# Performance work log

Measured on AMD Instinct MI355X. Metric: run time of the kernel, lower is better.

The kernel has to match this reference:

```python
import jax, jax.numpy as jnp
import numpy as np

N_NODES = 50000
N_EDGES = 800000
IN_C = 128
OUT_C = 128
NEG_SLOPE = 0.2  # leaky_relu alpha


def setup_inputs() -> dict:
    key = jax.random.key(0)
    k1, k2, k3, k4 = jax.random.split(key, 4)
    h = jax.random.normal(k1, (N_NODES, IN_C), dtype=jnp.float32)
    edge_index = jax.random.randint(k2, (2, N_EDGES), 0, N_NODES, dtype=jnp.int64)
    # xavier_uniform with gain=1.414
    gW = 1.414 * np.sqrt(6.0 / (IN_C + OUT_C))
    W = jax.random.uniform(k3, (IN_C, OUT_C), dtype=jnp.float32, minval=-gW, maxval=gW)
    ga = 1.414 * np.sqrt(6.0 / (2 * OUT_C + 1))
    a = jax.random.uniform(k4, (2 * OUT_C, 1), dtype=jnp.float32, minval=-ga, maxval=ga)
    return {"h": h, "edge_index": edge_index, "W": W, "a": a}


def reference(h, edge_index, W, a):
    # eval mode (no dropout), concat=True -> ELU output
    Wh = h @ W                                  # [N, F]
    row, col = edge_index[0], edge_index[1]     # source, target
    F_out = W.shape[1]
    # cat([Wh_i, Wh_j]) @ a  ==  (Wh @ a_src)[row] + (Wh @ a_dst)[col]
    alpha_src = Wh @ a[:F_out, 0]               # [N]
    alpha_dst = Wh @ a[F_out:, 0]               # [N]
    edge_e = jax.nn.leaky_relu(alpha_src[row] + alpha_dst[col], negative_slope=NEG_SLOPE)  # [E]
    n = Wh.shape[0]
    # segment softmax over incoming edges of each target node
    m = jax.ops.segment_max(edge_e, col, num_segments=n)       # [N] (-inf for empty, never indexed)
    exp_e = jnp.exp(edge_e - m[col])                            # [E]
    s = jax.ops.segment_sum(exp_e, col, num_segments=n)         # [N]
    attn = exp_e / (s[col] + 1e-16)                              # [E]
    # scatter-add aggregation of attended source features
    h_prime = jax.ops.segment_sum(Wh[row] * attn[:, None], col, num_segments=n)  # [N, F]
    return jax.nn.elu(h_prime)
```

## Files before the change

### kernel.cpp

```cpp
#include <hip/hip_runtime.h>
#include <math.h>

#define NEG_BIG -1.0e30f
#define BSHIFT 8
#define MAXB 256

typedef __attribute__((ext_vector_type(8))) short short8v;
typedef __attribute__((ext_vector_type(4))) float f32x4;

__device__ __forceinline__ ushort f2bf(float f) {
  unsigned u = __float_as_uint(f);
  unsigned r = (u + 0x7fffu + ((u >> 16) & 1u)) >> 16;
  return (ushort)r;
}
__device__ __forceinline__ float bf_lo(unsigned u) { return __uint_as_float(u << 16); }
__device__ __forceinline__ float bf_hi(unsigned u) { return __uint_as_float(u & 0xffff0000u); }

__global__ void wprep_k(const float* __restrict__ W, ushort* __restrict__ Wbf,
                        int* __restrict__ bucket_count, int* __restrict__ done) {
  int j = blockIdx.x * blockDim.x + threadIdx.x;
  if (j < MAXB) bucket_count[j] = 0;
  if (j == 0) *done = 0;
  if (j >= 128 * 128) return;
  int i = j & 7;
  int l = (j >> 3) & 63;
  int n0 = (j >> 9) & 7;
  int kk = j >> 12;
  int k = kk * 32 + ((l >> 4) & 3) * 8 + i;
  int n = n0 * 16 + (l & 15);
  Wbf[j] = f2bf(W[k * 128 + n]);
}

__global__ __launch_bounds__(256) void hist_gemm_k(
    const void* __restrict__ ei, int E,
    unsigned* __restrict__ packed, int* __restrict__ bucket_count,
    int* __restrict__ done, int* __restrict__ bcur, int* __restrict__ bucket_base,
    int hblocks,
    const float* __restrict__ h, const ushort* __restrict__ Wbf,
    const float* __restrict__ a, ushort* __restrict__ Whb,
    float* __restrict__ asrc, float* __restrict__ adst, int N) {
  __shared__ int lh[MAXB];
  __shared__ int wsum[4];
  __shared__ int last;
  int tid = (int)threadIdx.x;

  if ((int)blockIdx.x < hblocks) {
    lh[tid] = 0;
    __syncthreads();

    const int* p32 = (const int*)ei;
    bool is64 = true;
#pragma unroll
    for (int i = 0; i < 32; ++i) is64 = is64 && (p32[2 * i + 1] == 0);
    const long long* p64 = (const long long*)ei;
    int stride = hblocks * 256;
    for (int e = blockIdx.x * 256 + tid; e < E; e += stride) {
      int r, c;
      if (is64) { r = (int)p64[e]; c = (int)p64[E + e]; }
      else      { r = p32[e];      c = p32[E + e]; }
      packed[e] = ((unsigned)c << 16) | (unsigned)r;
      atomicAdd(&lh[c >> BSHIFT], 1);
    }
    __syncthreads();
    if (lh[tid]) atomicAdd(&bucket_count[tid], lh[tid]);
    __syncthreads();
    if (tid == 0) {
      __threadfence();
      int old = atomicAdd(done, 1);
      last = (old == hblocks - 1);
    }
    __syncthreads();
    if (!last) return;
    __threadfence();

    int lane = tid & 63, wid = tid >> 6;
    int v = atomicAdd(&bucket_count[tid], 0);
    int x = v;
#pragma unroll
    for (int off = 1; off < 64; off <<= 1) {
      int t = __shfl_up(x, off);
      if (lane >= off) x += t;
    }
    if (lane == 63) wsum[wid] = x;
    __syncthreads();
    int woff = 0;
    for (int w = 0; w < wid; ++w) woff += wsum[w];
    int excl = woff + x - v;
    bcur[tid] = excl;
    bucket_base[tid] = excl;
    if (tid == 255) bucket_base[256] = excl + v;
    return;
  }

  int gb = (int)blockIdx.x - hblocks;
  int w = tid >> 6;
  int l = tid & 63;
  int lg = l >> 4;
  int lm = l & 15;
  int r0 = gb * 64 + 16 * w;
  const short8v* Wb8 = (const short8v*)Wbf;

  float as_v[8], ad_v[8];
#pragma unroll
  for (int n0 = 0; n0 < 8; ++n0) {
    as_v[n0] = a[n0 * 16 + lm];
    ad_v[n0] = a[128 + n0 * 16 + lm];
  }

  f32x4 acc[8];
#pragma unroll
  for (int n0 = 0; n0 < 8; ++n0) acc[n0] = (f32x4){0.f, 0.f, 0.f, 0.f};

  int arow = r0 + lm;
  const float* hrow = h + (size_t)arow * 128;
  bool rok = (arow < N);

#pragma unroll
  for (int kk = 0; kk < 4; ++kk) {
    short8v av;
    if (rok) {
      const float4* hp = (const float4*)(hrow + kk * 32 + lg * 8);
      float4 x0 = hp[0], x1 = hp[1];
      av[0] = (short)f2bf(x0.x); av[1] = (short)f2bf(x0.y);
      av[2] = (short)f2bf(x0.z); av[3] = (short)f2bf(x0.w);
      av[4] = (short)f2bf(x1.x); av[5] = (short)f2bf(x1.y);
      av[6] = (short)f2bf(x1.z); av[7] = (short)f2bf(x1.w);
    } else {
      av = (short8v){0, 0, 0, 0, 0, 0, 0, 0};
    }
#pragma unroll
    for (int n0 = 0; n0 < 8; ++n0) {
      short8v bv = Wb8[(kk * 8 + n0) * 64 + l];
      acc[n0] = __builtin_amdgcn_mfma_f32_16x16x32_bf16(av, bv, acc[n0], 0, 0, 0);
    }
  }

#pragma unroll
  for (int reg = 0; reg < 4; ++reg) {
    int r = r0 + lg * 4 + reg;
    if (r < N) {
      short8v pk;
#pragma unroll
      for (int n0 = 0; n0 < 8; ++n0) pk[n0] = (short)f2bf(acc[n0][reg]);
      *(short8v*)(Whb + (size_t)r * 128 + lm * 8) = pk;
    }
  }

#pragma unroll
  for (int reg = 0; reg < 4; ++reg) {
    float ps = 0.f, pd = 0.f;
#pragma unroll
    for (int n0 = 0; n0 < 8; ++n0) {
      ps += acc[n0][reg] * as_v[n0];
      pd += acc[n0][reg] * ad_v[n0];
    }
#pragma unroll
    for (int off = 1; off < 16; off <<= 1) {
      ps += __shfl_xor(ps, off);
      pd += __shfl_xor(pd, off);
    }
    int r = r0 + lg * 4 + reg;
    if (lm == 0 && r < N) { asrc[r] = ps; adst[r] = pd; }
  }
}

#define TILE 8192
__global__ __launch_bounds__(1024) void bin_k(const unsigned* __restrict__ packed,
                                              int* __restrict__ bcur,
                                              unsigned* __restrict__ bin_buf, int E) {
  __shared__ int lhist[MAXB];
  __shared__ int lbase[MAXB];
  int tid = (int)threadIdx.x;
  int t0 = blockIdx.x * TILE;

  if (tid < MAXB) lhist[tid] = 0;
  __syncthreads();

  unsigned rec[8];
  int rb[8], rr[8];
#pragma unroll
  for (int k = 0; k < 8; ++k) {
    int i = t0 + tid + k * 1024;
    rb[k] = -1;
    if (i < E) {
      rec[k] = packed[i];
      rb[k] = (int)(rec[k] >> (16 + BSHIFT));
      rr[k] = atomicAdd(&lhist[rb[k]], 1);
    }
  }
  __syncthreads();
  if (tid < MAXB) lbase[tid] = lhist[tid] ? atomicAdd(&bcur[tid], lhist[tid]) : 0;
  __syncthreads();
#pragma unroll
  for (int k = 0; k < 8; ++k) {
    if (rb[k] >= 0) bin_buf[lbase[rb[k]] + rr[k]] = rec[k];
  }
}

__global__ __launch_bounds__(1024) void perm3_k(const unsigned* __restrict__ bin_buf,
                                                const int* __restrict__ bucket_base,
                                                int* __restrict__ rowptr,
                                                ushort* __restrict__ row_sorted,
                                                int N, int nbuckets) {
  __shared__ int hist[MAXB];
  __shared__ int cur[MAXB];
  __shared__ int wsum[16];
  int b = blockIdx.x;
  int tid = (int)threadIdx.x;
  int c0 = b << BSHIFT;
  int ncol = min(MAXB, N - c0);
  int e0 = bucket_base[b], e1 = bucket_base[b + 1];

  if (tid < MAXB) hist[tid] = 0;
  __syncthreads();
  for (int i = e0 + tid; i < e1; i += 1024) {
    int cl = (int)(bin_buf[i] >> 16) - c0;
    if ((unsigned)cl < (unsigned)MAXB) atomicAdd(&hist[cl], 1);
  }
  __syncthreads();

  int lane = tid & 63, wid = tid >> 6;
  int v = (tid < MAXB) ? hist[tid] : 0;
  int x = v;
#pragma unroll
  for (int off = 1; off < 64; off <<= 1) {
    int t = __shfl_up(x, off);
    if (lane >= off) x += t;
  }
  if (lane == 63) wsum[wid] = x;
  __syncthreads();
  if (tid < MAXB) {
    int woff = 0;
    for (int w = 0; w < wid; ++w) woff += wsum[w];
    int excl = woff + x - v;
    cur[tid] = e0 + excl;
    if (tid < ncol) rowptr[c0 + tid] = e0 + excl;
  }
  if (b == nbuckets - 1 && tid == 0) rowptr[N] = e1;
  __syncthreads();

  for (int i = e0 + tid; i < e1; i += 1024) {
    unsigned rec = bin_buf[i];
    int cl = (int)(rec >> 16) - c0;
    if ((unsigned)cl < (unsigned)MAXB) {
      int p = atomicAdd(&cur[cl], 1);
      row_sorted[p] = (ushort)(rec & 0xffffu);
    }
  }
}

__global__ __launch_bounds__(256) void softagg_k(const int* __restrict__ rowptr,
                                                 const ushort* __restrict__ row_sorted,
                                                 const float* __restrict__ asrc,
                                                 const float* __restrict__ adst,
                                                 const ushort* __restrict__ Whb,
                                                 float* __restrict__ out, int N) {
  int node = blockIdx.x * 4 + ((int)threadIdx.x >> 6);
  if (node >= N) return;
  int lane = (int)threadIdx.x & 63;
  int beg = rowptr[node], end = rowptr[node + 1];
  int deg = end - beg;
  float adc = adst[node];
  float ax = 0.f, ay = 0.f;

  if (deg <= 64) {
    int r = 0;
    float v = NEG_BIG;
    if (lane < deg) {
      r = row_sorted[beg + lane];
      v = asrc[r] + adc;
      v = (v >= 0.f) ? v : 0.2f * v;
    }
    float m = v;
#pragma unroll
    for (int off = 32; off > 0; off >>= 1) m = fmaxf(m, __shfl_xor(m, off));
    float e = (lane < deg) ? __expf(v - m) : 0.f;
    float s = e;
#pragma unroll
    for (int off = 32; off > 0; off >>= 1) s += __shfl_xor(s, off);
    float w = e / (s + 1e-16f);

    int j = 0;
    for (; j + 7 < deg; j += 8) {
      float wv[8];
      int rv[8];
#pragma unroll
      for (int q = 0; q < 8; ++q) { wv[q] = __shfl(w, j + q); rv[q] = __shfl(r, j + q); }
      unsigned u[8];
#pragma unroll
      for (int q = 0; q < 8; ++q) u[q] = ((const unsigned*)(Whb + (size_t)rv[q] * 128))[lane];
#pragma unroll
      for (int q = 0; q < 8; ++q) { ax += wv[q] * bf_lo(u[q]); ay += wv[q] * bf_hi(u[q]); }
    }
    for (; j < deg; ++j) {
      float wj = __shfl(w, j);
      int rj = __shfl(r, j);
      unsigned u = ((const unsigned*)(Whb + (size_t)rj * 128))[lane];
      ax += wj * bf_lo(u); ay += wj * bf_hi(u);
    }
  } else {
    float m = NEG_BIG, s = 0.f;
    for (int i = beg + lane; i < end; i += 64) {
      float v = asrc[row_sorted[i]] + adc;
      v = (v >= 0.f) ? v : 0.2f * v;
      if (v > m) { s = s * __expf(m - v) + 1.f; m = v; }
      else       { s += __expf(v - m); }
    }
#pragma unroll
    for (int off = 32; off > 0; off >>= 1) {
      float mo = __shfl_xor(m, off);
      float so = __shfl_xor(s, off);
      float M = fmaxf(m, mo);
      s = s * __expf(m - M) + so * __expf(mo - M);
      m = M;
    }
    float inv = 1.f / (s + 1e-16f);
    for (int i = beg; i < end; ++i) {
      int rj = row_sorted[i];
      float v = asrc[rj] + adc;
      v = (v >= 0.f) ? v : 0.2f * v;
      float wj = __expf(v - m) * inv;
      unsigned u = ((const unsigned*)(Whb + (size_t)rj * 128))[lane];
      ax += wj * bf_lo(u); ay += wj * bf_hi(u);
    }
  }

  ax = ax > 0.f ? ax : expm1f(ax);
  ay = ay > 0.f ? ay : expm1f(ay);
  int c0 = ((lane & 3) << 5) + (lane >> 2);
  float* orow = out + (size_t)node * 128;
  orow[c0] = ax;
  orow[c0 + 16] = ay;
}

extern "C" void kernel_launch(void* const* d_in, const int* in_sizes, int n_in,
                              void* d_out, int out_size, void* d_ws, size_t ws_size,
                              hipStream_t stream) {
  const float* h = (const float*)d_in[0];
  const void* ei = d_in[1];
  const float* W = (const float*)d_in[2];
  const float* a = (const float*)d_in[3];
  int N = in_sizes[0] / 128;
  int E = in_sizes[1] / 2;
  float* out = (float*)d_out;

  ushort* Whb = (ushort*)d_ws;
  float* asrc = (float*)(Whb + (size_t)N * 128);
  float* adst = asrc + N;
  int* bucket_count = (int*)(adst + N);
  int* done = bucket_count + MAXB;
  int* bcur = done + 4;
  int* bucket_base = bcur + MAXB;
  int* rowptr = bucket_base + MAXB + 4;
  unsigned* bin_buf = (unsigned*)(rowptr + N + 1);
  unsigned* packed = bin_buf + E;
  ushort* row_sorted = (ushort*)(packed + E);
  ushort* Wbf = row_sorted + E;

  int nbuckets = (N + MAXB - 1) >> BSHIFT;
  const int HBLOCKS = 256;
  int gblocks = (N + 63) / 64;

  wprep_k<<<64, 256, 0, stream>>>(W, Wbf, bucket_count, done);
  hist_gemm_k<<<HBLOCKS + gblocks, 256, 0, stream>>>(
      ei, E, packed, bucket_count, done, bcur, bucket_base, HBLOCKS,
      h, Wbf, a, Whb, asrc, adst, N);
  bin_k<<<(E + TILE - 1) / TILE, 1024, 0, stream>>>(packed, bcur, bin_buf, E);
  perm3_k<<<nbuckets, 1024, 0, stream>>>(bin_buf, bucket_base, rowptr, row_sorted, N, nbuckets);
  softagg_k<<<(N + 3) / 4, 256, 0, stream>>>(rowptr, row_sorted, asrc, adst, Whb, out, N);
}
```

Before: 90.29 us.

## Split GEMM blocks across histogram, binning and permute kernels to overlap work

Moves the dense h@W MFMA GEMM into a shared device function and divides its row blocks into three parts. Each part runs alongside one of the histogram, binning and permutation kernels, so the latency-bound sort stages share the GPU with compute work. The bin and permute kernels also drop from 1024 to 256 threads per block, with a smaller bin tile, so they launch more blocks. The risk is that GEMM blocks now compete with the sort blocks on each launch and lengthen those critical stages.

Measured after the change: 100.2 us. 11.0% more time.

```diff
diff --git a/kernel.cpp b/kernel.cpp
--- a/kernel.cpp
+++ b/kernel.cpp
@@ -15,6 +15,84 @@
 }
 __device__ __forceinline__ float bf_lo(unsigned u) { return __uint_as_float(u << 16); }
 __device__ __forceinline__ float bf_hi(unsigned u) { return __uint_as_float(u & 0xffff0000u); }
+
+__device__ __forceinline__ void gemm_body(int gb, const float* __restrict__ h,
+                                          const ushort* __restrict__ Wbf,
+                                          const float* __restrict__ a,
+                                          ushort* __restrict__ Whb,
+                                          float* __restrict__ asrc,
+                                          float* __restrict__ adst, int N) {
+  int tid = (int)threadIdx.x;
+  int w = tid >> 6;
+  int l = tid & 63;
+  int lg = l >> 4;
+  int lm = l & 15;
+  int r0 = gb * 64 + 16 * w;
+  const short8v* Wb8 = (const short8v*)Wbf;
+
+  float as_v[8], ad_v[8];
+#pragma unroll
+  for (int n0 = 0; n0 < 8; ++n0) {
+    as_v[n0] = a[n0 * 16 + lm];
+    ad_v[n0] = a[128 + n0 * 16 + lm];
+  }
+
+  f32x4 acc[8];
+#pragma unroll
+  for (int n0 = 0; n0 < 8; ++n0) acc[n0] = (f32x4){0.f, 0.f, 0.f, 0.f};
+
+  int arow = r0 + lm;
+  const float* hrow = h + (size_t)arow * 128;
+  bool rok = (arow < N);
+
+#pragma unroll
+  for (int kk = 0; kk < 4; ++kk) {
+    short8v av;
+    if (rok) {
+      const float4* hp = (const float4*)(hrow + kk * 32 + lg * 8);
+      float4 x0 = hp[0], x1 = hp[1];
+      av[0] = (short)f2bf(x0.x); av[1] = (short)f2bf(x0.y);
+      av[2] = (short)f2bf(x0.z); av[3] = (short)f2bf(x0.w);
+      av[4] = (short)f2bf(x1.x); av[5] = (short)f2bf(x1.y);
+      av[6] = (short)f2bf(x1.z); av[7] = (short)f2bf(x1.w);
+    } else {
+      av = (short8v){0, 0, 0, 0, 0, 0, 0, 0};
+    }
+#pragma unroll
+    for (int n0 = 0; n0 < 8; ++n0) {
+      short8v bv = Wb8[(kk * 8 + n0) * 64 + l];
+      acc[n0] = __builtin_amdgcn_mfma_f32_16x16x32_bf16(av, bv, acc[n0], 0, 0, 0);
+    }
+  }
+
+#pragma unroll
+  for (int reg = 0; reg < 4; ++reg) {
+    int r = r0 + lg * 4 + reg;
+    if (r < N) {
+      short8v pk;
+#pragma unroll
+      for (int n0 = 0; n0 < 8; ++n0) pk[n0] = (short)f2bf(acc[n0][reg]);
+      *(short8v*)(Whb + (size_t)r * 128 + lm * 8) = pk;
+    }
+  }
+
+#pragma unroll
+  for (int reg = 0; reg < 4; ++reg) {
+    float ps = 0.f, pd = 0.f;
+#pragma unroll
+    for (int n0 = 0; n0 < 8; ++n0) {
+      ps += acc[n0][reg] * as_v[n0];
+      pd += acc[n0][reg] * ad_v[n0];
+    }
+#pragma unroll
+    for (int off = 1; off < 16; off <<= 1) {
+      ps += __shfl_xor(ps, off);
+      pd += __shfl_xor(pd, off);
+    }
+    int r = r0 + lg * 4 + reg;
+    if (lm == 0 && r < N) { asrc[r] = ps; adst[r] = pd; }
+  }
+}
 
 __global__ void wprep_k(const float* __restrict__ W, ushort* __restrict__ Wbf,
                         int* __restrict__ bucket_count, int* __restrict__ done) {
@@ -38,149 +116,88 @@
     int hblocks,
     const float* __restrict__ h, const ushort* __restrict__ Wbf,
     const float* __restrict__ a, ushort* __restrict__ Whb,
-    float* __restrict__ asrc, float* __restrict__ adst, int N) {
+    float* __restrict__ asrc, float* __restrict__ adst, int N, int gb0) {
   __shared__ int lh[MAXB];
   __shared__ int wsum[4];
   __shared__ int last;
   int tid = (int)threadIdx.x;
 
-  if ((int)blockIdx.x < hblocks) {
-    lh[tid] = 0;
-    __syncthreads();
-
-    const int* p32 = (const int*)ei;
-    bool is64 = true;
-#pragma unroll
-    for (int i = 0; i < 32; ++i) is64 = is64 && (p32[2 * i + 1] == 0);
-    const long long* p64 = (const long long*)ei;
-    int stride = hblocks * 256;
-    for (int e = blockIdx.x * 256 + tid; e < E; e += stride) {
-      int r, c;
-      if (is64) { r = (int)p64[e]; c = (int)p64[E + e]; }
-      else      { r = p32[e];      c = p32[E + e]; }
-      packed[e] = ((unsigned)c << 16) | (unsigned)r;
-      atomicAdd(&lh[c >> BSHIFT], 1);
-    }
-    __syncthreads();
-    if (lh[tid]) atomicAdd(&bucket_count[tid], lh[tid]);
-    __syncthreads();
-    if (tid == 0) {
-      __threadfence();
-      int old = atomicAdd(done, 1);
-      last = (old == hblocks - 1);
-    }
-    __syncthreads();
-    if (!last) return;
+  if ((int)blockIdx.x >= hblocks) {
+    gemm_body((int)blockIdx.x - hblocks + gb0, h, Wbf, a, Whb, asrc, adst, N);
+    return;
+  }
+
+  lh[tid] = 0;
+  __syncthreads();
+
+  const int* p32 = (const int*)ei;
+  bool is64 = true;
+#pragma unroll
+  for (int i = 0; i < 32; ++i) is64 = is64 && (p32[2 * i + 1] == 0);
+  const long long* p64 = (const long long*)ei;
+  int stride = hblocks * 256;
+  for (int e = blockIdx.x * 256 + tid; e < E; e += stride) {
+    int r, c;
+    if (is64) { r = (int)p64[e]; c = (int)p64[E + e]; }
+    else      { r = p32[e];      c = p32[E + e]; }
+    packed[e] = ((unsigned)c << 16) | (unsigned)r;
+    atomicAdd(&lh[c >> BSHIFT], 1);
+  }
+  __syncthreads();
+  if (lh[tid]) atomicAdd(&bucket_count[tid], lh[tid]);
+  __syncthreads();
+  if (tid == 0) {
     __threadfence();
-
-    int lane = tid & 63, wid = tid >> 6;
-    int v = atomicAdd(&bucket_count[tid], 0);
-    int x = v;
-#pragma unroll
-    for (int off = 1; off < 64; off <<= 1) {
-      int t = __shfl_up(x, off);
-      if (lane >= off) x += t;
-    }
-    if (lane == 63) wsum[wid] = x;
-    __syncthreads();
-    int woff = 0;
-    for (int w = 0; w < wid; ++w) woff += wsum[w];
-    int excl = woff + x - v;
-    bcur[tid] = excl;
-    bucket_base[tid] = excl;
-    if (tid == 255) bucket_base[256] = excl + v;
-    return;
-  }
-
-  int gb = (int)blockIdx.x - hblocks;
-  int w = tid >> 6;
-  int l = tid & 63;
-  int lg = l >> 4;
-  int lm = l & 15;
-  int r0 = gb * 64 + 16 * w;
-  const short8v* Wb8 = (const short8v*)Wbf;
-
-  float as_v[8], ad_v[8];
-#pragma unroll
-  for (int n0 = 0; n0 < 8; ++n0) {
-    as_v[n0] = a[n0 * 16 + lm];
-    ad_v[n0] = a[128 + n0 * 16 + lm];
-  }
-
-  f32x4 acc[8];
-#pragma unroll
-  for (int n0 = 0; n0 < 8; ++n0) acc[n0] = (f32x4){0.f, 0.f, 0.f, 0.f};
-
-  int arow = r0 + lm;
-  const float* hrow = h + (size_t)arow * 128;
-  bool rok = (arow < N);
-
-#pragma unroll
-  for (int kk = 0; kk < 4; ++kk) {
-    short8v av;
-    if (rok) {
-      const float4* hp = (const float4*)(hrow + kk * 32 + lg * 8);
-      float4 x0 = hp[0], x1 = hp[1];
-      av[0] = (short)f2bf(x0.x); av[1] = (short)f2bf(x0.y);
-      av[2] = (short)f2bf(x0.z); av[3] = (short)f2bf(x0.w);
-      av[4] = (short)f2bf(x1.x); av[5] = (short)f2bf(x1.y);
-      av[6] = (short)f2bf(x1.z); av[7] = (short)f2bf(x1.w);
-    } else {
-      av = (short8v){0, 0, 0, 0, 0, 0, 0, 0};
-    }
-#pragma unroll
-    for (int n0 = 0; n0 < 8; ++n0) {
-      short8v bv = Wb8[(kk * 8 + n0) * 64 + l];
-      acc[n0] = __builtin_amdgcn_mfma_f32_16x16x32_bf16(av, bv, acc[n0], 0, 0, 0);
-    }
-  }
-
-#pragma unroll
-  for (int reg = 0; reg < 4; ++reg) {
-    int r = r0 + lg * 4 + reg;
-    if (r < N) {
-      short8v pk;
-#pragma unroll
-      for (int n0 = 0; n0 < 8; ++n0) pk[n0] = (short)f2bf(acc[n0][reg]);
-      *(short8v*)(Whb + (size_t)r * 128 + lm * 8) = pk;
-    }
-  }
-
-#pragma unroll
-  for (int reg = 0; reg < 4; ++reg) {
-    float ps = 0.f, pd = 0.f;
-#pragma unroll
-    for (int n0 = 0; n0 < 8; ++n0) {
-      ps += acc[n0][reg] * as_v[n0];
-      pd += acc[n0][reg] * ad_v[n0];
-    }
-#pragma unroll
-    for (int off = 1; off < 16; off <<= 1) {
-      ps += __shfl_xor(ps, off);
-      pd += __shfl_xor(pd, off);
-    }
-    int r = r0 + lg * 4 + reg;
-    if (lm == 0 && r < N) { asrc[r] = ps; adst[r] = pd; }
-  }
-}
-
-#define TILE 8192
-__global__ __launch_bounds__(1024) void bin_k(const unsigned* __restrict__ packed,
-                                              int* __restrict__ bcur,
-                                              unsigned* __restrict__ bin_buf, int E) {
+    int old = atomicAdd(done, 1);
+    last = (old == hblocks - 1);
+  }
+  __syncthreads();
+  if (!last) return;
+  __threadfence();
+
+  int lane = tid & 63, wid = tid >> 6;
+  int v = atomicAdd(&bucket_count[tid], 0);
+  int x = v;
+#pragma unroll
+  for (int off = 1; off < 64; off <<= 1) {
+    int t = __shfl_up(x, off);
+    if (lane >= off) x += t;
+  }
+  if (lane == 63) wsum[wid] = x;
+  __syncthreads();
+  int woff = 0;
+  for (int w = 0; w < wid; ++w) woff += wsum[w];
+  int excl = woff + x - v;
+  bcur[tid] = excl;
+  bucket_base[tid] = excl;
+  if (tid == 255) bucket_base[256] = excl + v;
+}
+
+#define TILE2 2048
+__global__ __launch_bounds__(256) void bin_gemm_k(
+    const unsigned* __restrict__ packed, int* __restrict__ bcur,
+    unsigned* __restrict__ bin_buf, int E, int eblk,
+    const float* __restrict__ h, const ushort* __restrict__ Wbf,
+    const float* __restrict__ a, ushort* __restrict__ Whb,
+    float* __restrict__ asrc, float* __restrict__ adst, int N, int gb0) {
   __shared__ int lhist[MAXB];
   __shared__ int lbase[MAXB];
   int tid = (int)threadIdx.x;
-  int t0 = blockIdx.x * TILE;
-
-  if (tid < MAXB) lhist[tid] = 0;
+
+  if ((int)blockIdx.x >= eblk) {
+    gemm_body((int)blockIdx.x - eblk + gb0, h, Wbf, a, Whb, asrc, adst, N);
+    return;
+  }
+
+  int t0 = blockIdx.x * TILE2;
+  lhist[tid] = 0;
   __syncthreads();
 
   unsigned rec[8];
   int rb[8], rr[8];
 #pragma unroll
   for (int k = 0; k < 8; ++k) {
-    int i = t0 + tid + k * 1024;
+    int i = t0 + tid + k * 256;
     rb[k] = -1;
     if (i < E) {
       rec[k] = packed[i];
@@ -189,7 +206,7 @@
     }
   }
   __syncthreads();
-  if (tid < MAXB) lbase[tid] = lhist[tid] ? atomicAdd(&bcur[tid], lhist[tid]) : 0;
+  lbase[tid] = lhist[tid] ? atomicAdd(&bcur[tid], lhist[tid]) : 0;
   __syncthreads();
 #pragma unroll
   for (int k = 0; k < 8; ++k) {
@@ -197,30 +214,37 @@
   }
 }
 
-__global__ __launch_bounds__(1024) void perm3_k(const unsigned* __restrict__ bin_buf,
-                                                const int* __restrict__ bucket_base,
-                                                int* __restrict__ rowptr,
-                                                ushort* __restrict__ row_sorted,
-                                                int N, int nbuckets) {
+__global__ __launch_bounds__(256) void perm_gemm_k(
+    const unsigned* __restrict__ bin_buf, const int* __restrict__ bucket_base,
+    int* __restrict__ rowptr, ushort* __restrict__ row_sorted, int nbuckets,
+    const float* __restrict__ h, const ushort* __restrict__ Wbf,
+    const float* __restrict__ a, ushort* __restrict__ Whb,
+    float* __restrict__ asrc, float* __restrict__ adst, int N, int gb0) {
   __shared__ int hist[MAXB];
   __shared__ int cur[MAXB];
-  __shared__ int wsum[16];
-  int b = blockIdx.x;
+  __shared__ int wsum[4];
   int tid = (int)threadIdx.x;
+
+  if ((int)blockIdx.x >= nbuckets) {
+    gemm_body((int)blockIdx.x - nbuckets + gb0, h, Wbf, a, Whb, asrc, adst, N);
+    return;
+  }
+
+  int b = (int)blockIdx.x;
   int c0 = b << BSHIFT;
   int ncol = min(MAXB, N - c0);
   int e0 = bucket_base[b], e1 = bucket_base[b + 1];
 
-  if (tid < MAXB) hist[tid] = 0;
-  __syncthreads();
-  for (int i = e0 + tid; i < e1; i += 1024) {
+  hist[tid] = 0;
+  __syncthreads();
+  for (int i = e0 + tid; i < e1; i += 256) {
     int cl = (int)(bin_buf[i] >> 16) - c0;
     if ((unsigned)cl < (unsigned)MAXB) atomicAdd(&hist[cl], 1);
   }
   __syncthreads();
 
   int lane = tid & 63, wid = tid >> 6;
-  int v = (tid < MAXB) ? hist[tid] : 0;
+  int v = hist[tid];
   int x = v;
 #pragma unroll
   for (int off = 1; off < 64; off <<= 1) {
@@ -229,17 +253,15 @@
   }
   if (lane == 63) wsum[wid] = x;
   __syncthreads();
-  if (tid < MAXB) {
-    int woff = 0;
-    for (int w = 0; w < wid; ++w) woff += wsum[w];
-    int excl = woff + x - v;
-    cur[tid] = e0 + excl;
-    if (tid < ncol) rowptr[c0 + tid] = e0 + excl;
-  }
-  if (b == nbuckets - 1 && tid == 0) rowptr[N] = e1;
-  __syncthreads();
-
-  for (int i = e0 + tid; i < e1; i += 1024) {
+  int woff = 0;
+  for (int w = 0; w < wid; ++w) woff += wsum[w];
+  int excl = woff + x - v;
+  cur[tid] = e0 + excl;
+  if (tid < ncol) rowptr[c0 + tid] = e0 + excl;
+  if (b == nbuckets - 1 && tid == 0) rowptr[c0 + ncol] = e1;
+  __syncthreads();
+
+  for (int i = e0 + tid; i < e1; i += 256) {
     unsigned rec = bin_buf[i];
     int cl = (int)(rec >> 16) - c0;
     if ((unsigned)cl < (unsigned)MAXB) {
@@ -359,13 +381,21 @@
 
   int nbuckets = (N + MAXB - 1) >> BSHIFT;
   const int HBLOCKS = 256;
-  int gblocks = (N + 63) / 64;
+  int eblk = (E + TILE2 - 1) / TILE2;
+  int gtot = (N + 63) / 64;
+  int G1 = gtot / 3;
+  int G2 = (gtot - G1) / 2;
+  int G3 = gtot - G1 - G2;
 
   wprep_k<<<64, 256, 0, stream>>>(W, Wbf, bucket_count, done);
-  hist_gemm_k<<<HBLOCKS + gblocks, 256, 0, stream>>>(
+  hist_gemm_k<<<HBLOCKS + G1, 256, 0, stream>>>(
       ei, E, packed, bucket_count, done, bcur, bucket_base, HBLOCKS,
-      h, Wbf, a, Whb, asrc, adst, N);
-  bin_k<<<(E + TILE - 1) / TILE, 1024, 0, stream>>>(packed, bcur, bin_buf, E);
-  perm3_k<<<nbuckets, 1024, 0, stream>>>(bin_buf, bucket_base, rowptr, row_sorted, N, nbuckets);
+      h, Wbf, a, Whb, asrc, adst, N, 0);
+  bin_gemm_k<<<eblk + G2, 256, 0, stream>>>(
+      packed, bcur, bin_buf, E, eblk,
+      h, Wbf, a, Whb, asrc, adst, N, G1);
+  perm_gemm_k<<<nbuckets + G3, 256, 0, stream>>>(
+      bin_buf, bucket_base, rowptr, row_sorted, nbuckets,
+      h, Wbf, a, Whb, asrc, adst, N, G1 + G2);
   softagg_k<<<(N + 3) / 4, 256, 0, stream>>>(rowptr, row_sorted, asrc, adst, Whb, out, N);
 }
```

## Split node GEMM across hist, bin and perm kernels to fill idle CUs

Applied to the files above, without the earlier changes.

The dense h@W GEMM (with the attention projections) is factored into a device helper, and its row tiles are split in three parts. One third runs alongside the histogram blocks as before, and the other two parts are appended as extra blocks to the binning and permutation kernels. The aim is to fill the CUs left idle by the small bin/perm grids (about 98 and 196 blocks), so that this work hides the GEMM cost. The catch is that the extra 1024-thread GEMM blocks could lengthen those kernels or raise register pressure, since they share one launch bound.

Result: slower. 95.53 us (+5.8%).

```diff
diff --git a/kernel.cpp b/kernel.cpp
--- a/kernel.cpp
+++ b/kernel.cpp
@@ -15,6 +15,83 @@
 }
 __device__ __forceinline__ float bf_lo(unsigned u) { return __uint_as_float(u << 16); }
 __device__ __forceinline__ float bf_hi(unsigned u) { return __uint_as_float(u & 0xffff0000u); }
+
+__device__ __forceinline__ void gemm_waves(int base, const float* __restrict__ h,
+                                           const ushort* __restrict__ Wbf,
+                                           const float* __restrict__ a,
+                                           ushort* __restrict__ Whb,
+                                           float* __restrict__ asrc,
+                                           float* __restrict__ adst, int N) {
+  int tid = (int)threadIdx.x;
+  int l = tid & 63;
+  int lg = l >> 4;
+  int lm = l & 15;
+  int r0 = base + 16 * (tid >> 6);
+  const short8v* Wb8 = (const short8v*)Wbf;
+
+  float as_v[8], ad_v[8];
+#pragma unroll
+  for (int n0 = 0; n0 < 8; ++n0) {
+    as_v[n0] = a[n0 * 16 + lm];
+    ad_v[n0] = a[128 + n0 * 16 + lm];
+  }
+
+  f32x4 acc[8];
+#pragma unroll
+  for (int n0 = 0; n0 < 8; ++n0) acc[n0] = (f32x4){0.f, 0.f, 0.f, 0.f};
+
+  int arow = r0 + lm;
+  const float* hrow = h + (size_t)arow * 128;
+  bool rok = (arow < N);
+
+#pragma unroll
+  for (int kk = 0; kk < 4; ++kk) {
+    short8v av;
+    if (rok) {
+      const float4* hp = (const float4*)(hrow + kk * 32 + lg * 8);
+      float4 x0 = hp[0], x1 = hp[1];
+      av[0] = (short)f2bf(x0.x); av[1] = (short)f2bf(x0.y);
+      av[2] = (short)f2bf(x0.z); av[3] = (short)f2bf(x0.w);
+      av[4] = (short)f2bf(x1.x); av[5] = (short)f2bf(x1.y);
+      av[6] = (short)f2bf(x1.z); av[7] = (short)f2bf(x1.w);
+    } else {
+      av = (short8v){0, 0, 0, 0, 0, 0, 0, 0};
+    }
+#pragma unroll
+    for (int n0 = 0; n0 < 8; ++n0) {
+      short8v bv = Wb8[(kk * 8 + n0) * 64 + l];
+      acc[n0] = __builtin_amdgcn_mfma_f32_16x16x32_bf16(av, bv, acc[n0], 0, 0, 0);
+    }
+  }
+
+#pragma unroll
+  for (int reg = 0; reg < 4; ++reg) {
+    int r = r0 + lg * 4 + reg;
+    if (r < N) {
+      short8v pk;
+#pragma unroll
+      for (int n0 = 0; n0 < 8; ++n0) pk[n0] = (short)f2bf(acc[n0][reg]);
+      *(short8v*)(Whb + (size_t)r * 128 + lm * 8) = pk;
+    }
+  }
+
+#pragma unroll
+  for (int reg = 0; reg < 4; ++reg) {
+    float ps = 0.f, pd = 0.f;
+#pragma unroll
+    for (int n0 = 0; n0 < 8; ++n0) {
+      ps += acc[n0][reg] * as_v[n0];
+      pd += acc[n0][reg] * ad_v[n0];
+    }
+#pragma unroll
+    for (int off = 1; off < 16; off <<= 1) {
+      ps += __shfl_xor(ps, off);
+      pd += __shfl_xor(pd, off);
+    }
+    int r = r0 + lg * 4 + reg;
+    if (lm == 0 && r < N) { asrc[r] = ps; adst[r] = pd; }
+  }
+}
 
 __global__ void wprep_k(const float* __restrict__ W, ushort* __restrict__ Wbf,
                         int* __restrict__ bucket_count, int* __restrict__ done) {
@@ -44,135 +121,74 @@
   __shared__ int last;
   int tid = (int)threadIdx.x;
 
-  if ((int)blockIdx.x < hblocks) {
-    lh[tid] = 0;
-    __syncthreads();
-
-    const int* p32 = (const int*)ei;
-    bool is64 = true;
-#pragma unroll
-    for (int i = 0; i < 32; ++i) is64 = is64 && (p32[2 * i + 1] == 0);
-    const long long* p64 = (const long long*)ei;
-    int stride = hblocks * 256;
-    for (int e = blockIdx.x * 256 + tid; e < E; e += stride) {
-      int r, c;
-      if (is64) { r = (int)p64[e]; c = (int)p64[E + e]; }
-      else      { r = p32[e];      c = p32[E + e]; }
-      packed[e] = ((unsigned)c << 16) | (unsigned)r;
-      atomicAdd(&lh[c >> BSHIFT], 1);
-    }
-    __syncthreads();
-    if (lh[tid]) atomicAdd(&bucket_count[tid], lh[tid]);
-    __syncthreads();
-    if (tid == 0) {
-      __threadfence();
-      int old = atomicAdd(done, 1);
-      last = (old == hblocks - 1);
-    }
-    __syncthreads();
-    if (!last) return;
+  if ((int)blockIdx.x >= hblocks) {
+    gemm_waves(((int)blockIdx.x - hblocks) * 64, h, Wbf, a, Whb, asrc, adst, N);
+    return;
+  }
+
+  lh[tid] = 0;
+  __syncthreads();
+
+  const int* p32 = (const int*)ei;
+  bool is64 = true;
+#pragma unroll
+  for (int i = 0; i < 32; ++i) is64 = is64 && (p32[2 * i + 1] == 0);
+  const long long* p64 = (const long long*)ei;
+  int stride = hblocks * 256;
+  for (int e = blockIdx.x * 256 + tid; e < E; e += stride) {
+    int r, c;
+    if (is64) { r = (int)p64[e]; c = (int)p64[E + e]; }
+    else      { r = p32[e];      c = p32[E + e]; }
+    packed[e] = ((unsigned)c << 16) | (unsigned)r;
+    atomicAdd(&lh[c >> BSHIFT], 1);
+  }
+  __syncthreads();
+  if (lh[tid]) atomicAdd(&bucket_count[tid], lh[tid]);
+  __syncthreads();
+  if (tid == 0) {
     __threadfence();
-
-    int lane = tid & 63, wid = tid >> 6;
-    int v = atomicAdd(&bucket_count[tid], 0);
-    int x = v;
-#pragma unroll
-    for (int off = 1; off < 64; off <<= 1) {
-      int t = __shfl_up(x, off);
-      if (lane >= off) x += t;
-    }
-    if (lane == 63) wsum[wid] = x;
-    __syncthreads();
-    int woff = 0;
-    for (int w = 0; w < wid; ++w) woff += wsum[w];
-    int excl = woff + x - v;
-    bcur[tid] = excl;
-    bucket_base[tid] = excl;
-    if (tid == 255) bucket_base[256] = excl + v;
-    return;
-  }
-
-  int gb = (int)blockIdx.x - hblocks;
-  int w = tid >> 6;
-  int l = tid & 63;
-  int lg = l >> 4;
-  int lm = l & 15;
-  int r0 = gb * 64 + 16 * w;
-  const short8v* Wb8 = (const short8v*)Wbf;
-
-  float as_v[8], ad_v[8];
-#pragma unroll
-  for (int n0 = 0; n0 < 8; ++n0) {
-    as_v[n0] = a[n0 * 16 + lm];
-    ad_v[n0] = a[128 + n0 * 16 + lm];
-  }
-
-  f32x4 acc[8];
-#pragma unroll
-  for (int n0 = 0; n0 < 8; ++n0) acc[n0] = (f32x4){0.f, 0.f, 0.f, 0.f};
-
-  int arow = r0 + lm;
-  const float* hrow = h + (size_t)arow * 128;
-  bool rok = (arow < N);
-
-#pragma unroll
-  for (int kk = 0; kk < 4; ++kk) {
-    short8v av;
-    if (rok) {
-      const float4* hp = (const float4*)(hrow + kk * 32 + lg * 8);
-      float4 x0 = hp[0], x1 = hp[1];
-      av[0] = (short)f2bf(x0.x); av[1] = (short)f2bf(x0.y);
-      av[2] = (short)f2bf(x0.z); av[3] = (short)f2bf(x0.w);
-      av[4] = (short)f2bf(x1.x); av[5] = (short)f2bf(x1.y);
-      av[6] = (short)f2bf(x1.z); av[7] = (short)f2bf(x1.w);
-    } else {
-      av = (short8v){0, 0, 0, 0, 0, 0, 0, 0};
-    }
-#pragma unroll
-    for (int n0 = 0; n0 < 8; ++n0) {
-      short8v bv = Wb8[(kk * 8 + n0) * 64 + l];
-      acc[n0] = __builtin_amdgcn_mfma_f32_16x16x32_bf16(av, bv, acc[n0], 0, 0, 0);
-    }
-  }
-
-#pragma unroll
-  for (int reg = 0; reg < 4; ++reg) {
-    int r = r0 + lg * 4 + reg;
-    if (r < N) {
-      short8v pk;
-#pragma unroll
-      for (int n0 = 0; n0 < 8; ++n0) pk[n0] = (short)f2bf(acc[n0][reg]);
-      *(short8v*)(Whb + (size_t)r * 128 + lm * 8) = pk;
-    }
-  }
-
-#pragma unroll
-  for (int reg = 0; reg < 4; ++reg) {
-    float ps = 0.f, pd = 0.f;
-#pragma unroll
-    for (int n0 = 0; n0 < 8; ++n0) {
-      ps += acc[n0][reg] * as_v[n0];
-      pd += acc[n0][reg] * ad_v[n0];
-    }
-#pragma unroll
-    for (int off = 1; off < 16; off <<= 1) {
-      ps += __shfl_xor(ps, off);
-      pd += __shfl_xor(pd, off);
-    }
-    int r = r0 + lg * 4 + reg;
-    if (lm == 0 && r < N) { asrc[r] = ps; adst[r] = pd; }
-  }
+    int old = atomicAdd(done, 1);
+    last = (old == hblocks - 1);
+  }
+  __syncthreads();
+  if (!last) return;
+  __threadfence();
+
+  int lane = tid & 63, wid = tid >> 6;
+  int v = atomicAdd(&bucket_count[tid], 0);
+  int x = v;
+#pragma unroll
+  for (int off = 1; off < 64; off <<= 1) {
+    int t = __shfl_up(x, off);
+    if (lane >= off) x += t;
+  }
+  if (lane == 63) wsum[wid] = x;
+  __syncthreads();
+  int woff = 0;
+  for (int w = 0; w < wid; ++w) woff += wsum[w];
+  int excl = woff + x - v;
+  bcur[tid] = excl;
+  bucket_base[tid] = excl;
+  if (tid == 255) bucket_base[256] = excl + v;
 }
 
 #define TILE 8192
-__global__ __launch_bounds__(1024) void bin_k(const unsigned* __restrict__ packed,
-                                              int* __restrict__ bcur,
-                                              unsigned* __restrict__ bin_buf, int E) {
+__global__ __launch_bounds__(1024) void bin_gemm_k(
+    const unsigned* __restrict__ packed, int* __restrict__ bcur,
+    unsigned* __restrict__ bin_buf, int E, int eblk,
+    const float* __restrict__ h, const ushort* __restrict__ Wbf,
+    const float* __restrict__ a, ushort* __restrict__ Whb,
+    float* __restrict__ asrc, float* __restrict__ adst, int N, int gbase) {
   __shared__ int lhist[MAXB];
   __shared__ int lbase[MAXB];
   int tid = (int)threadIdx.x;
+
+  if ((int)blockIdx.x >= eblk) {
+    gemm_waves(gbase + ((int)blockIdx.x - eblk) * 256, h, Wbf, a, Whb, asrc, adst, N);
+    return;
+  }
+
   int t0 = blockIdx.x * TILE;
-
   if (tid < MAXB) lhist[tid] = 0;
   __syncthreads();
 
@@ -197,16 +213,23 @@
   }
 }
 
-__global__ __launch_bounds__(1024) void perm3_k(const unsigned* __restrict__ bin_buf,
-                                                const int* __restrict__ bucket_base,
-                                                int* __restrict__ rowptr,
-                                                ushort* __restrict__ row_sorted,
-                                                int N, int nbuckets) {
+__global__ __launch_bounds__(1024) void perm_gemm_k(
+    const unsigned* __restrict__ bin_buf, const int* __restrict__ bucket_base,
+    int* __restrict__ rowptr, ushort* __restrict__ row_sorted, int N, int nbuckets,
+    const float* __restrict__ h, const ushort* __restrict__ Wbf,
+    const float* __restrict__ a, ushort* __restrict__ Whb,
+    float* __restrict__ asrc, float* __restrict__ adst, int gbase) {
   __shared__ int hist[MAXB];
   __shared__ int cur[MAXB];
   __shared__ int wsum[16];
-  int b = blockIdx.x;
   int tid = (int)threadIdx.x;
+
+  if ((int)blockIdx.x >= nbuckets) {
+    gemm_waves(gbase + ((int)blockIdx.x - nbuckets) * 256, h, Wbf, a, Whb, asrc, adst, N);
+    return;
+  }
+
+  int b = (int)blockIdx.x;
   int c0 = b << BSHIFT;
   int ncol = min(MAXB, N - c0);
   int e0 = bucket_base[b], e1 = bucket_base[b + 1];
@@ -359,13 +382,26 @@
 
   int nbuckets = (N + MAXB - 1) >> BSHIFT;
   const int HBLOCKS = 256;
-  int gblocks = (N + 63) / 64;
+  int eblk = (E + TILE - 1) / TILE;
+
+  int gtiles = (N + 63) / 64;
+  int t1 = gtiles / 3;
+  int rows_rem = (gtiles - t1) * 64;
+  int nb34 = (rows_rem + 255) / 256;
+  int nb3 = (nb34 + 1) / 2;
+  int nb4 = nb34 - nb3;
+  int base3 = t1 * 64;
+  int base4 = base3 + nb3 * 256;
 
   wprep_k<<<64, 256, 0, stream>>>(W, Wbf, bucket_count, done);
-  hist_gemm_k<<<HBLOCKS + gblocks, 256, 0, stream>>>(
+  hist_gemm_k<<<HBLOCKS + t1, 256, 0, stream>>>(
       ei, E, packed, bucket_count, done, bcur, bucket_base, HBLOCKS,
       h, Wbf, a, Whb, asrc, adst, N);
-  bin_k<<<(E + TILE - 1) / TILE, 1024, 0, stream>>>(packed, bcur, bin_buf, E);
-  perm3_k<<<nbuckets, 1024, 0, stream>>>(bin_buf, bucket_base, rowptr, row_sorted, N, nbuckets);
+  bin_gemm_k<<<eblk + nb3, 1024, 0, stream>>>(
+      packed, bcur, bin_buf, E, eblk,
+      h, Wbf, a, Whb, asrc, adst, N, base3);
+  perm_gemm_k<<<nbuckets + nb4, 1024, 0, stream>>>(
+      bin_buf, bucket_base, rowptr, row_sorted, N, nbuckets,
+      h, Wbf, a, Whb, asrc, adst, base4);
   softagg_k<<<(N + 3) / 4, 256, 0, stream>>>(rowptr, row_sorted, asrc, adst, Whb, out, N);
 }
```
